# Kernel optimization log

Measured on AMD Instinct MI355X. Metric: run time of the kernel, lower is better.

Reference implementation:

```python
import jax, jax.numpy as jnp
import numpy as np

OVERLAP_THRESHOLD = 0.5
NEG_POS_RATIO = 3
ALPHA = 1.0


def cxcy_to_xy(cxcy):
    return jnp.concatenate([cxcy[..., :2] - cxcy[..., 2:] / 2,
                            cxcy[..., :2] + cxcy[..., 2:] / 2], axis=-1)


def xy_to_cxcy(xy):
    return jnp.concatenate([(xy[..., :2] + xy[..., 2:]) / 2,
                            xy[..., 2:] - xy[..., :2]], axis=-1)


def cxcy_to_gcxgcy(cxcy, priors_cxcy):
    return jnp.concatenate([
        (cxcy[..., :2] - priors_cxcy[..., :2]) / (priors_cxcy[..., 2:] / 10.0),
        jnp.log(cxcy[..., 2:] / priors_cxcy[..., 2:]) * 5.0], axis=-1)


def jaccard(a, b):
    # a: [N,4] xy, b: [P,4] xy -> [N,P]
    lo = jnp.maximum(a[:, None, :2], b[None, :, :2])
    hi = jnp.minimum(a[:, None, 2:], b[None, :, 2:])
    inter = jnp.prod(jnp.clip(hi - lo, 0.0), axis=-1)  # [N,P]
    area_a = jnp.prod(a[:, 2:] - a[:, :2], axis=-1)  # [N]
    area_b = jnp.prod(b[:, 2:] - b[:, :2], axis=-1)  # [P]
    return inter / (area_a[:, None] + area_b[None, :] - inter)


def _match_one(boxes_i, labels_i, priors_cxcy, priors_xy):
    n_objects = boxes_i.shape[0]
    overlap = jaccard(boxes_i, priors_xy)  # [N,P]
    overlap_for_each_prior = overlap.max(axis=0)  # [P]
    object_for_each_prior = overlap.argmax(axis=0)  # [P]
    prior_for_each_object = overlap.argmax(axis=1)  # [N]
    # force each object to own its best prior
    object_for_each_prior = object_for_each_prior.at[prior_for_each_object].set(
        jnp.arange(n_objects))
    overlap_for_each_prior = overlap_for_each_prior.at[prior_for_each_object].set(1.0)
    labels_for_each_prior = labels_i[object_for_each_prior]
    labels_for_each_prior = jnp.where(overlap_for_each_prior < OVERLAP_THRESHOLD,
                                      0, labels_for_each_prior)
    matched = boxes_i[object_for_each_prior]  # [P,4]
    true_locs = cxcy_to_gcxgcy(xy_to_cxcy(matched), priors_cxcy)  # [P,4]
    return true_locs, labels_for_each_prior


def reference(predicted_locs, predicted_scores, boxes, labels, priors_cxcy):
    B, P, C = predicted_scores.shape
    priors_xy = cxcy_to_xy(priors_cxcy)
    true_locs, true_classes = jax.vmap(
        _match_one, in_axes=(0, 0, None, None))(boxes, labels, priors_cxcy, priors_xy)
    # true_locs: [B,P,4], true_classes: [B,P]
    positive = true_classes != 0  # [B,P]
    n_pos = positive.sum(axis=1)  # [B]
    n_pos_total = n_pos.sum()

    # SmoothL1 (beta=1, mean over selected elements = n_pos_total*4)
    d = predicted_locs - true_locs
    ad = jnp.abs(d)
    sl1 = jnp.where(ad < 1.0, 0.5 * d * d, ad - 0.5)  # [B,P,4]
    loc_loss = (sl1 * positive[..., None]).sum() / (n_pos_total.astype(jnp.float32) * 4.0)

    # per-prior cross-entropy
    logp = jax.nn.log_softmax(predicted_scores, axis=-1)  # [B,P,C]
    conf_all = -jnp.take_along_axis(logp, true_classes[..., None], axis=-1)[..., 0]  # [B,P]

    conf_pos_sum = jnp.where(positive, conf_all, 0.0).sum()
    conf_neg = jnp.where(positive, 0.0, conf_all)
    conf_neg_sorted = jnp.sort(conf_neg, axis=1)[:, ::-1]  # descending
    n_hard_neg = NEG_POS_RATIO * n_pos  # [B]
    rank = jnp.arange(P)[None, :]
    hard_neg_mask = rank < n_hard_neg[:, None]
    conf_hard_neg_sum = jnp.where(hard_neg_mask, conf_neg_sorted, 0.0).sum()

    conf_loss = (conf_hard_neg_sum + conf_pos_sum) / n_pos_total.astype(jnp.float32)
    return conf_loss + ALPHA * loc_loss


def setup_inputs() -> dict:
    key = jax.random.key(0)
    ks = jax.random.split(key, 7)
    B, P, C, N = 128, 8732, 21, 16
    predicted_locs = jax.random.normal(ks[0], (B, P, 4), dtype=jnp.float32)
    predicted_scores = jax.random.normal(ks[1], (B, P, C), dtype=jnp.float32)
    # valid xy boxes in [0,1]
    p1 = jax.random.uniform(ks[2], (B, N, 2)) * 0.85
    wh = jax.random.uniform(ks[3], (B, N, 2), minval=0.02, maxval=0.15)
    boxes = jnp.concatenate([p1, jnp.minimum(p1 + wh, 1.0)], axis=-1)
    labels = jax.random.randint(ks[4], (B, N), 1, C)
    cxcy = jax.random.uniform(ks[5], (P, 2))
    pwh = jax.random.uniform(ks[6], (P, 2), minval=0.05, maxval=0.5)
    priors_cxcy = jnp.concatenate([cxcy, pwh], axis=-1)
    return {"predicted_locs": predicted_locs, "predicted_scores": predicted_scores,
            "boxes": boxes, "labels": labels, "priors_cxcy": priors_cxcy}
```

## Files before the change

### kernel.cpp

```cpp
#include <hip/hip_runtime.h>


#define MAXN 16
#define MAXE 16
#define SPLIT 8

__device__ __forceinline__ float sl1f(float d) {
    float ad = fabsf(d);
    return ad < 1.0f ? 0.5f * d * d : ad - 0.5f;
}

__global__ __launch_bounds__(256) void k_pre(
    const float* __restrict__ boxes,
    const float* __restrict__ priors,
    int P, int N,
    float* __restrict__ pf_in,
    float* __restrict__ pf_un,
    int*   __restrict__ pf_id,
    int* __restrict__ npos,
    float* __restrict__ acc)
{
    __shared__ float sbx1[MAXN], sby1[MAXN], sbx2[MAXN], sby2[MAXN], sba[MAXN];
    __shared__ float win[4][MAXN], wun[4][MAXN];
    __shared__ int   widd[4][MAXN];
    const int id = blockIdx.x;
    const int tid = threadIdx.x;
    const int lane = tid & 63, w = tid >> 6;
    const int b = id / SPLIT, s = id % SPLIT;

    if (s == 0 && tid == 0) npos[b] = 0;
    if (id == 0 && tid < 2) ((unsigned*)acc)[tid] = 0u;
    if (N > MAXN) N = MAXN;

    if (tid < N) {
        const float* bp = boxes + ((size_t)b * N + tid) * 4;
        float x1 = bp[0], y1 = bp[1], x2 = bp[2], y2 = bp[3];
        sbx1[tid] = x1; sby1[tid] = y1; sbx2[tid] = x2; sby2[tid] = y2;
        sba[tid] = (x2 - x1) * (y2 - y1);
    }
    __syncthreads();

    float rx1[MAXN], ry1[MAXN], rx2[MAXN], ry2[MAXN], rar[MAXN];
#pragma unroll
    for (int n = 0; n < MAXN; n++) {
        if (n < N) { rx1[n]=sbx1[n]; ry1[n]=sby1[n]; rx2[n]=sbx2[n]; ry2[n]=sby2[n]; rar[n]=sba[n]; }
        else       { rx1[n]=0.f; ry1[n]=0.f; rx2[n]=0.f; ry2[n]=0.f; rar[n]=0.f; }
    }

    const int Q = (P + SPLIT - 1) / SPLIT;
    const int pbeg = s * Q;
    const int pend = min(pbeg + Q, P);

    float bi[MAXN], bu[MAXN]; int bx[MAXN];
#pragma unroll
    for (int n = 0; n < MAXN; n++) { bi[n] = -1.0f; bu[n] = 1.0f; bx[n] = 0x7fffffff; }

    for (int p = pbeg + tid; p < pend; p += 256) {
        float4 pr = ((const float4*)priors)[p];
        float px1 = pr.x - pr.z * 0.5f, py1 = pr.y - pr.w * 0.5f;
        float px2 = pr.x + pr.z * 0.5f, py2 = pr.y + pr.w * 0.5f;
        float parea = (px2 - px1) * (py2 - py1);
#pragma unroll
        for (int n = 0; n < MAXN; n++) {
            if (n < N) {
                float iw = fmaxf(fminf(rx2[n], px2) - fmaxf(rx1[n], px1), 0.0f);
                float ih = fmaxf(fminf(ry2[n], py2) - fmaxf(ry1[n], py1), 0.0f);
                float in = iw * ih;
                float un = rar[n] + parea - in;
                if (in * bu[n] > bi[n] * un) { bi[n] = in; bu[n] = un; bx[n] = p; }
            }
        }
    }

#pragma unroll
    for (int n = 0; n < MAXN; n++) {
        if (n < N) {
#pragma unroll
            for (int off = 32; off > 0; off >>= 1) {
                float oin = __shfl_down(bi[n], off);
                float oun = __shfl_down(bu[n], off);
                int   oid = __shfl_down(bx[n], off);
                float a = oin * bu[n], c = bi[n] * oun;
                if (a > c || (a == c && oid < bx[n])) { bi[n] = oin; bu[n] = oun; bx[n] = oid; }
            }
            if (lane == 0) { win[w][n] = bi[n]; wun[w][n] = bu[n]; widd[w][n] = bx[n]; }
        }
    }
    __syncthreads();
    if (tid < N) {
        const int n = tid;
        float fi = win[0][n], fu = wun[0][n]; int fx = widd[0][n];
        for (int ww = 1; ww < 4; ww++) {
            float oin = win[ww][n], oun = wun[ww][n]; int oid = widd[ww][n];
            float a = oin * fu, c = fi * oun;
            if (a > c || (a == c && oid < fx)) { fi = oin; fu = oun; fx = oid; }
        }
        const size_t o = ((size_t)b * SPLIT + s) * MAXN + n;
        pf_in[o] = fi; pf_un[o] = fu; pf_id[o] = fx;
    }
}

template<int CT>
__global__ __launch_bounds__(256) void k_fused(
    const float* __restrict__ plocs,
    const float* __restrict__ scores,
    const float* __restrict__ boxes,
    const int*   __restrict__ labels,
    const float* __restrict__ priors,
    const float* __restrict__ pf_in,
    const float* __restrict__ pf_un,
    const int*   __restrict__ pf_id,
    int P, int Crt, int N, int nchunk,
    float* __restrict__ conf_out,
    int*   __restrict__ npos,
    float* __restrict__ locpart,
    float* __restrict__ pospart)
{
    const int C = CT > 0 ? CT : Crt;
    extern __shared__ float sh[];
    __shared__ float sx1[MAXN], sy1[MAXN], sx2[MAXN], sy2[MAXN], barea[MAXN];
    __shared__ int   blab[MAXN], spfo[MAXN];
    __shared__ float redf[4], redp[4];
    __shared__ int   redi[4];

    const int b = blockIdx.y;
    const int tid = threadIdx.x;
    const int lane = tid & 63, wid = tid >> 6;
    if (N > MAXN) N = MAXN;
    const int p0 = blockIdx.x * 256;
    const int rows = min(256, P - p0);

    if (tid < N) {
        const float* bp = boxes + ((size_t)b * N + tid) * 4;
        float x1 = bp[0], y1 = bp[1], x2 = bp[2], y2 = bp[3];
        sx1[tid] = x1; sy1[tid] = y1; sx2[tid] = x2; sy2[tid] = y2;
        barea[tid] = (x2 - x1) * (y2 - y1);
        blab[tid] = labels[(size_t)b * N + tid];
        const size_t base = (size_t)b * SPLIT * MAXN + tid;
        float fi = pf_in[base], fu = pf_un[base]; int fx = pf_id[base];
#pragma unroll
        for (int sp = 1; sp < SPLIT; sp++) {
            float oin = pf_in[base + (size_t)sp * MAXN];
            float oun = pf_un[base + (size_t)sp * MAXN];
            int   oid = pf_id[base + (size_t)sp * MAXN];
            if (oin * fu > fi * oun) { fi = oin; fu = oun; fx = oid; }
        }
        spfo[tid] = fx;
    }

    {
        const size_t f4base = ((size_t)b * P + p0) * C / 4;
        const int f4cnt = (rows * C + 3) / 4;
        const float4* __restrict__ s4 = (const float4*)scores + f4base;
        if ((P & 3) == 0) {
            for (int c = wid; c * 64 < f4cnt; c += 4) {
                int idx = c * 64 + lane;
                if (idx < f4cnt) {
                    __builtin_amdgcn_global_load_lds(
                        (const __attribute__((address_space(1))) void*)(s4 + idx),
                        (__attribute__((address_space(3))) void*)((char*)sh + (size_t)c * 1024),
                        16, 0, 0);
                }
            }
            asm volatile("s_waitcnt vmcnt(0)" ::: "memory");
        } else {
            for (int j = tid; j < f4cnt; j += 256)
                ((float4*)sh)[j] = s4[j];
        }
    }
    __syncthreads();

    const int p = p0 + tid;
    float locs = 0.0f, posc = 0.0f, conf = 0.0f;
    int np = 0;
    if (p < P) {
        float4 pr = ((const float4*)priors)[p];
        float px1 = pr.x - pr.z * 0.5f, py1 = pr.y - pr.w * 0.5f;
        float px2 = pr.x + pr.z * 0.5f, py2 = pr.y + pr.w * 0.5f;
        float parea = (px2 - px1) * (py2 - py1);
        float bi = -1.0f, bu = 1.0f; int bestn = 0;
#pragma unroll
        for (int n = 0; n < MAXN; n++) {
            if (n < N) {
                float iw = fmaxf(fminf(sx2[n], px2) - fmaxf(sx1[n], px1), 0.0f);
                float ih = fmaxf(fminf(sy2[n], py2) - fmaxf(sy1[n], py1), 0.0f);
                float in = iw * ih;
                float un = barea[n] + parea - in;
                if (in * bu > bi * un) { bi = in; bu = un; bestn = n; }
            }
        }
#pragma unroll
        for (int n = 0; n < MAXN; n++) {
            if (n < N && spfo[n] == p) { bestn = n; bi = 1.0f; bu = 1.0f; }
        }
        const int lab = (bi < 0.5f * bu) ? 0 : blab[bestn];

        const float* r = sh + tid * C;
        float m = -3.402823466e38f;
#pragma unroll
        for (int c = 0; c < C; c++) m = fmaxf(m, r[c]);
        float sum = 0.0f;
#pragma unroll
        for (int c = 0; c < C; c++) sum += __expf(r[c] - m);
        float ce = m + __logf(sum) - r[lab];

        if (lab != 0) {
            posc = ce; np = 1;
            int n = bestn;
            float cx = (sx1[n] + sx2[n]) * 0.5f, cy = (sy1[n] + sy2[n]) * 0.5f;
            float w = sx2[n] - sx1[n], h = sy2[n] - sy1[n];
            float g0 = (cx - pr.x) / (pr.z / 10.0f);
            float g1 = (cy - pr.y) / (pr.w / 10.0f);
            float g2 = logf(w / pr.z) * 5.0f;
            float g3 = logf(h / pr.w) * 5.0f;
            float4 pl = ((const float4*)plocs)[(size_t)b * P + p];
            locs = sl1f(pl.x - g0) + sl1f(pl.y - g1) + sl1f(pl.z - g2) + sl1f(pl.w - g3);
        } else {
            conf = ce;
        }
        conf_out[(size_t)b * P + p] = conf;
    }
#pragma unroll
    for (int off = 32; off > 0; off >>= 1) {
        locs += __shfl_down(locs, off);
        posc += __shfl_down(posc, off);
        np   += __shfl_down(np, off);
    }
    if (lane == 0) { redf[wid] = locs; redp[wid] = posc; redi[wid] = np; }
    __syncthreads();
    if (tid == 0) {
        float L = redf[0] + redf[1] + redf[2] + redf[3];
        float Pp = redp[0] + redp[1] + redp[2] + redp[3];
        int   c = redi[0] + redi[1] + redi[2] + redi[3];
        if (c) atomicAdd(&npos[b], c);
        locpart[b * nchunk + blockIdx.x] = L;
        pospart[b * nchunk + blockIdx.x] = Pp;
    }
}

__global__ __launch_bounds__(1024, 4) void k_hard(
    const float* __restrict__ conf,
    const int* __restrict__ npos,
    const float* __restrict__ locpart,
    const float* __restrict__ pospart,
    int P, int B, int nloc,
    float* __restrict__ acc,
    float* __restrict__ out)
{
    __shared__ int   redi[2][16 * 3];
    __shared__ float redf2[16];
    __shared__ int   redi2[16];
    __shared__ float rl[16], rp[16];
    __shared__ int   rn[16], is_last;
    const int b = blockIdx.x, tid = threadIdx.x;
    const int lane = tid & 63, wid = tid >> 6;
    const int nthr = blockDim.x, nw = nthr >> 6;
    const int ne = (P + nthr - 1) / nthr;
    long long kk = (long long)npos[b] * 3;
    int k = kk > P ? P : (int)kk;

    float S = 0.0f;
    if (k > 0) {
        unsigned e[MAXE];
#pragma unroll
        for (int j = 0; j < MAXE; j++) {
            int p = j * nthr + tid;
            e[j] = (j < ne && p < P) ? __float_as_uint(conf[(size_t)b * P + p]) : 0u;
        }

        unsigned lo = 0u, hi = 0x7F800000u;
        int itp = 0;
        while (lo < hi) {
            int* buf = redi[itp & 1]; itp++;
            unsigned span = hi - lo;
            if (span >= 8) {
                unsigned q = span >> 2;
                unsigned m1 = lo + q, m2 = lo + 2 * q, m3 = lo + 3 * q;
                int c1 = 0, c2 = 0, c3 = 0;
#pragma unroll
                for (int j = 0; j < MAXE; j++) {
                    if (j < ne) {
                        unsigned v = e[j];
                        c1 += (int)__popcll(__ballot(v >= m1));
                        c2 += (int)__popcll(__ballot(v >= m2));
                        c3 += (int)__popcll(__ballot(v >= m3));
                    }
                }
                if (lane == 0) {
                    buf[wid * 3 + 0] = c1; buf[wid * 3 + 1] = c2; buf[wid * 3 + 2] = c3;
                }
                __syncthreads();
                int C1 = 0, C2 = 0, C3 = 0;
                for (int w = 0; w < nw; w++) {
                    C1 += buf[w * 3 + 0]; C2 += buf[w * 3 + 1]; C3 += buf[w * 3 + 2];
                }
                if      (C3 >= k) lo = m3;
                else if (C2 >= k) { lo = m2; hi = m3 - 1; }
                else if (C1 >= k) { lo = m1; hi = m2 - 1; }
                else              hi = m1 - 1;
            } else {
                unsigned mid = lo + ((span + 1) >> 1);
                int c = 0;
#pragma unroll
                for (int j = 0; j < MAXE; j++)
                    if (j < ne) c += (int)__popcll(__ballot(e[j] >= mid));
                if (lane == 0) buf[wid * 3] = c;
                __syncthreads();
                int Cc = 0;
                for (int w = 0; w < nw; w++) Cc += buf[w * 3];
                if (Cc >= k) lo = mid; else hi = mid - 1;
            }
        }
        __syncthreads();

        float t = __uint_as_float(lo);
        float sgt = 0.0f; int cgt = 0;
#pragma unroll
        for (int j = 0; j < MAXE; j++) {
            if (j < ne) {
                float v = __uint_as_float(e[j]);
                if (v > t) { sgt += v; cgt++; }
            }
        }
#pragma unroll
        for (int off = 32; off > 0; off >>= 1) {
            sgt += __shfl_down(sgt, off);
            cgt += __shfl_down(cgt, off);
        }
        if (lane == 0) { redf2[wid] = sgt; redi2[wid] = cgt; }
        __syncthreads();
        if (tid == 0) {
            int Cg = 0;
            for (int w = 0; w < nw; w++) { S += redf2[w]; Cg += redi2[w]; }
            S += (float)(k - Cg) * t;
        }
        __syncthreads();
    }

    if (tid == 0) {
        atomicAdd(&acc[0], S);
        __threadfence();
        unsigned tk = atomicAdd((unsigned*)(acc + 1), 1u);
        is_last = (tk == (unsigned)gridDim.x - 1) ? 1 : 0;
    }
    __syncthreads();
    if (is_last) {
        float lp = 0.0f, pp = 0.0f; int np = 0;
        for (int i = tid; i < nloc; i += nthr) { lp += locpart[i]; pp += pospart[i]; }
        for (int i = tid; i < B; i += nthr) np += npos[i];
#pragma unroll
        for (int off = 32; off > 0; off >>= 1) {
            lp += __shfl_down(lp, off);
            pp += __shfl_down(pp, off);
            np += __shfl_down(np, off);
        }
        if (lane == 0) { rl[wid] = lp; rp[wid] = pp; rn[wid] = np; }
        __syncthreads();
        if (tid == 0) {
            float L = 0.0f, Pp = 0.0f; int Np = 0;
            for (int w = 0; w < nw; w++) { L += rl[w]; Pp += rp[w]; Np += rn[w]; }
            float hard = atomicAdd(&acc[0], 0.0f);
            float npf = (float)Np;
            out[0] = (hard + Pp) / npf + L / (npf * 4.0f);
        }
    }
}

extern "C" void kernel_launch(void* const* d_in, const int* in_sizes, int n_in,
                              void* d_out, int out_size, void* d_ws, size_t ws_size,
                              hipStream_t stream)
{
    const float* plocs  = (const float*)d_in[0];
    const float* scores = (const float*)d_in[1];
    const float* boxes  = (const float*)d_in[2];
    const int*   labels = (const int*)d_in[3];
    const float* priors = (const float*)d_in[4];

    int P = in_sizes[4] / 4;
    int B = in_sizes[0] / (P * 4);
    int C = in_sizes[1] / (in_sizes[0] / 4);
    int N = in_sizes[3] / B;
    int nchunk = (P + 255) / 256;
    int nloc = B * nchunk;

    char* w = (char*)d_ws;
    float* slot    = (float*)w;  w += (size_t)B * P * sizeof(float);
    int*   npos    = (int*)w;    w += (size_t)B * sizeof(int);
    float* pf_in   = (float*)w;  w += (size_t)B * SPLIT * MAXN * sizeof(float);
    float* pf_un   = (float*)w;  w += (size_t)B * SPLIT * MAXN * sizeof(float);
    int*   pf_id   = (int*)w;    w += (size_t)B * SPLIT * MAXN * sizeof(int);
    float* locpart = (float*)w;  w += (size_t)nloc * sizeof(float);
    float* pospart = (float*)w;  w += (size_t)nloc * sizeof(float);
    w = (char*)(((uintptr_t)w + 63) & ~(uintptr_t)63);
    float* acc     = (float*)w;

    k_pre<<<B * SPLIT, 256, 0, stream>>>(boxes, priors, P, N,
                                         pf_in, pf_un, pf_id, npos, acc);

    dim3 ga(nchunk, B);
    size_t smf = (size_t)256 * C * sizeof(float);
    if (C == 21) {
        k_fused<21><<<ga, 256, smf, stream>>>(plocs, scores, boxes, labels, priors,
                                              pf_in, pf_un, pf_id, P, C, N, nchunk,
                                              slot, npos, locpart, pospart);
    } else {
        k_fused<0><<<ga, 256, smf, stream>>>(plocs, scores, boxes, labels, priors,
                                             pf_in, pf_un, pf_id, P, C, N, nchunk,
                                             slot, npos, locpart, pospart);
    }

    k_hard<<<B, 1024, 0, stream>>>(slot, npos, locpart, pospart,
                                   P, B, nloc, acc, (float*)d_out);
}
```

Before: 231.3 us.

## Repartition prior-matching kernel across object pairs and prior halves

The prior-matching pre-kernel now parallelises over pairs of objects and two halves of the priors instead of all 16 objects across 8 prior splits. Each block keeps only 2 boxes in registers, which cuts register pressure and raises the block count from B*8 to B*16. The fused kernel now merges 2 partial results per object instead of 8. Separately, the hard-negative threshold search drops its double-buffered reduction scratch in favour of one buffer with an extra barrier per iteration, which adds synchronisation cost.

```diff
diff --git a/kernel.cpp b/kernel.cpp
--- a/kernel.cpp
+++ b/kernel.cpp
@@ -3,7 +3,8 @@
 
 #define MAXN 16
 #define MAXE 16
-#define SPLIT 8
+#define KP_NB 2
+#define KP_SP 2
 
 __device__ __forceinline__ float sl1f(float d) {
     float ad = fabsf(d);
@@ -13,90 +14,87 @@
 __global__ __launch_bounds__(256) void k_pre(
     const float* __restrict__ boxes,
     const float* __restrict__ priors,
-    int P, int N,
+    int P, int N, int npair,
     float* __restrict__ pf_in,
     float* __restrict__ pf_un,
     int*   __restrict__ pf_id,
     int* __restrict__ npos,
     float* __restrict__ acc)
 {
-    __shared__ float sbx1[MAXN], sby1[MAXN], sbx2[MAXN], sby2[MAXN], sba[MAXN];
-    __shared__ float win[4][MAXN], wun[4][MAXN];
-    __shared__ int   widd[4][MAXN];
+    __shared__ float win[4][KP_NB], wun[4][KP_NB];
+    __shared__ int   widd[4][KP_NB];
     const int id = blockIdx.x;
     const int tid = threadIdx.x;
     const int lane = tid & 63, w = tid >> 6;
-    const int b = id / SPLIT, s = id % SPLIT;
-
-    if (s == 0 && tid == 0) npos[b] = 0;
+    const int per_b = npair * KP_SP;
+    const int b = id / per_b, rem = id % per_b;
+    const int pr = rem / KP_SP, h = rem % KP_SP;
+    const int n0 = pr * KP_NB;
+    const int nb = min(KP_NB, N - n0);
+
+    if (tid == 0 && rem == 0) npos[b] = 0;
     if (id == 0 && tid < 2) ((unsigned*)acc)[tid] = 0u;
-    if (N > MAXN) N = MAXN;
-
-    if (tid < N) {
-        const float* bp = boxes + ((size_t)b * N + tid) * 4;
-        float x1 = bp[0], y1 = bp[1], x2 = bp[2], y2 = bp[3];
-        sbx1[tid] = x1; sby1[tid] = y1; sbx2[tid] = x2; sby2[tid] = y2;
-        sba[tid] = (x2 - x1) * (y2 - y1);
+
+    float rx1[KP_NB], ry1[KP_NB], rx2[KP_NB], ry2[KP_NB], rar[KP_NB];
+#pragma unroll
+    for (int j = 0; j < KP_NB; j++) {
+        const int n = n0 + (j < nb ? j : 0);
+        const float* bp = boxes + ((size_t)b * N + n) * 4;
+        rx1[j] = bp[0]; ry1[j] = bp[1]; rx2[j] = bp[2]; ry2[j] = bp[3];
+        rar[j] = (rx2[j] - rx1[j]) * (ry2[j] - ry1[j]);
+    }
+
+    const int Q = (P + KP_SP - 1) / KP_SP;
+    const int pbeg = h * Q;
+    const int pend = min(pbeg + Q, P);
+
+    float bi[KP_NB], bu[KP_NB]; int bx[KP_NB];
+#pragma unroll
+    for (int j = 0; j < KP_NB; j++) { bi[j] = -1.0f; bu[j] = 1.0f; bx[j] = 0x7fffffff; }
+
+#pragma unroll 2
+    for (int p = pbeg + tid; p < pend; p += 256) {
+        float4 prr = ((const float4*)priors)[p];
+        float px1 = prr.x - prr.z * 0.5f, py1 = prr.y - prr.w * 0.5f;
+        float px2 = prr.x + prr.z * 0.5f, py2 = prr.y + prr.w * 0.5f;
+        float parea = (px2 - px1) * (py2 - py1);
+#pragma unroll
+        for (int j = 0; j < KP_NB; j++) {
+            float iw = fmaxf(fminf(rx2[j], px2) - fmaxf(rx1[j], px1), 0.0f);
+            float ih = fmaxf(fminf(ry2[j], py2) - fmaxf(ry1[j], py1), 0.0f);
+            float in = iw * ih;
+            float un = rar[j] + parea - in;
+            if (in * bu[j] > bi[j] * un) { bi[j] = in; bu[j] = un; bx[j] = p; }
+        }
+    }
+
+#pragma unroll
+    for (int j = 0; j < KP_NB; j++) {
+#pragma unroll
+        for (int off = 32; off > 0; off >>= 1) {
+            float oin = __shfl_down(bi[j], off);
+            float oun = __shfl_down(bu[j], off);
+            int   oid = __shfl_down(bx[j], off);
+            float a = oin * bu[j], c = bi[j] * oun;
+            if (a > c || (a == c && oid < bx[j])) { bi[j] = oin; bu[j] = oun; bx[j] = oid; }
+        }
+        if (lane == 0) { win[w][j] = bi[j]; wun[w][j] = bu[j]; widd[w][j] = bx[j]; }
     }
     __syncthreads();
-
-    float rx1[MAXN], ry1[MAXN], rx2[MAXN], ry2[MAXN], rar[MAXN];
-#pragma unroll
-    for (int n = 0; n < MAXN; n++) {
-        if (n < N) { rx1[n]=sbx1[n]; ry1[n]=sby1[n]; rx2[n]=sbx2[n]; ry2[n]=sby2[n]; rar[n]=sba[n]; }
-        else       { rx1[n]=0.f; ry1[n]=0.f; rx2[n]=0.f; ry2[n]=0.f; rar[n]=0.f; }
-    }
-
-    const int Q = (P + SPLIT - 1) / SPLIT;
-    const int pbeg = s * Q;
-    const int pend = min(pbeg + Q, P);
-
-    float bi[MAXN], bu[MAXN]; int bx[MAXN];
-#pragma unroll
-    for (int n = 0; n < MAXN; n++) { bi[n] = -1.0f; bu[n] = 1.0f; bx[n] = 0x7fffffff; }
-
-    for (int p = pbeg + tid; p < pend; p += 256) {
-        float4 pr = ((const float4*)priors)[p];
-        float px1 = pr.x - pr.z * 0.5f, py1 = pr.y - pr.w * 0.5f;
-        float px2 = pr.x + pr.z * 0.5f, py2 = pr.y + pr.w * 0.5f;
-        float parea = (px2 - px1) * (py2 - py1);
-#pragma unroll
-        for (int n = 0; n < MAXN; n++) {
-            if (n < N) {
-                float iw = fmaxf(fminf(rx2[n], px2) - fmaxf(rx1[n], px1), 0.0f);
-                float ih = fmaxf(fminf(ry2[n], py2) - fmaxf(ry1[n], py1), 0.0f);
-                float in = iw * ih;
-                float un = rar[n] + parea - in;
-                if (in * bu[n] > bi[n] * un) { bi[n] = in; bu[n] = un; bx[n] = p; }
-            }
-        }
-    }
-
-#pragma unroll
-    for (int n = 0; n < MAXN; n++) {
-        if (n < N) {
-#pragma unroll
-            for (int off = 32; off > 0; off >>= 1) {
-                float oin = __shfl_down(bi[n], off);
-                float oun = __shfl_down(bu[n], off);
-                int   oid = __shfl_down(bx[n], off);
-                float a = oin * bu[n], c = bi[n] * oun;
-                if (a > c || (a == c && oid < bx[n])) { bi[n] = oin; bu[n] = oun; bx[n] = oid; }
-            }
-            if (lane == 0) { win[w][n] = bi[n]; wun[w][n] = bu[n]; widd[w][n] = bx[n]; }
-        }
-    }
-    __syncthreads();
-    if (tid < N) {
-        const int n = tid;
-        float fi = win[0][n], fu = wun[0][n]; int fx = widd[0][n];
-        for (int ww = 1; ww < 4; ww++) {
-            float oin = win[ww][n], oun = wun[ww][n]; int oid = widd[ww][n];
-            float a = oin * fu, c = fi * oun;
-            if (a > c || (a == c && oid < fx)) { fi = oin; fu = oun; fx = oid; }
-        }
-        const size_t o = ((size_t)b * SPLIT + s) * MAXN + n;
-        pf_in[o] = fi; pf_un[o] = fu; pf_id[o] = fx;
+    if (tid == 0) {
+#pragma unroll
+        for (int j = 0; j < KP_NB; j++) {
+            float fi = win[0][j], fu = wun[0][j]; int fx = widd[0][j];
+            for (int ww = 1; ww < 4; ww++) {
+                float oin = win[ww][j], oun = wun[ww][j]; int oid = widd[ww][j];
+                float a = oin * fu, c = fi * oun;
+                if (a > c || (a == c && oid < fx)) { fi = oin; fu = oun; fx = oid; }
+            }
+            if (j < nb) {
+                const size_t o = ((size_t)b * KP_SP + h) * MAXN + n0 + j;
+                pf_in[o] = fi; pf_un[o] = fu; pf_id[o] = fx;
+            }
+        }
     }
 }
 
@@ -136,10 +134,10 @@
         sx1[tid] = x1; sy1[tid] = y1; sx2[tid] = x2; sy2[tid] = y2;
         barea[tid] = (x2 - x1) * (y2 - y1);
         blab[tid] = labels[(size_t)b * N + tid];
-        const size_t base = (size_t)b * SPLIT * MAXN + tid;
+        const size_t base = (size_t)b * KP_SP * MAXN + tid;
         float fi = pf_in[base], fu = pf_un[base]; int fx = pf_id[base];
 #pragma unroll
-        for (int sp = 1; sp < SPLIT; sp++) {
+        for (int sp = 1; sp < KP_SP; sp++) {
             float oin = pf_in[base + (size_t)sp * MAXN];
             float oun = pf_un[base + (size_t)sp * MAXN];
             int   oid = pf_id[base + (size_t)sp * MAXN];
@@ -247,7 +245,7 @@
     float* __restrict__ acc,
     float* __restrict__ out)
 {
-    __shared__ int   redi[2][16 * 3];
+    __shared__ int   redi[16 * 3];
     __shared__ float redf2[16];
     __shared__ int   redi2[16];
     __shared__ float rl[16], rp[16];
@@ -269,9 +267,7 @@
         }
 
         unsigned lo = 0u, hi = 0x7F800000u;
-        int itp = 0;
         while (lo < hi) {
-            int* buf = redi[itp & 1]; itp++;
             unsigned span = hi - lo;
             if (span >= 8) {
                 unsigned q = span >> 2;
@@ -287,13 +283,14 @@
                     }
                 }
                 if (lane == 0) {
-                    buf[wid * 3 + 0] = c1; buf[wid * 3 + 1] = c2; buf[wid * 3 + 2] = c3;
+                    redi[wid * 3 + 0] = c1; redi[wid * 3 + 1] = c2; redi[wid * 3 + 2] = c3;
                 }
                 __syncthreads();
                 int C1 = 0, C2 = 0, C3 = 0;
                 for (int w = 0; w < nw; w++) {
-                    C1 += buf[w * 3 + 0]; C2 += buf[w * 3 + 1]; C3 += buf[w * 3 + 2];
+                    C1 += redi[w * 3 + 0]; C2 += redi[w * 3 + 1]; C3 += redi[w * 3 + 2];
                 }
+                __syncthreads();
                 if      (C3 >= k) lo = m3;
                 else if (C2 >= k) { lo = m2; hi = m3 - 1; }
                 else if (C1 >= k) { lo = m1; hi = m2 - 1; }
@@ -304,14 +301,14 @@
 #pragma unroll
                 for (int j = 0; j < MAXE; j++)
                     if (j < ne) c += (int)__popcll(__ballot(e[j] >= mid));
-                if (lane == 0) buf[wid * 3] = c;
+                if (lane == 0) redi[wid * 3] = c;
                 __syncthreads();
                 int Cc = 0;
-                for (int w = 0; w < nw; w++) Cc += buf[w * 3];
+                for (int w = 0; w < nw; w++) Cc += redi[w * 3];
+                __syncthreads();
                 if (Cc >= k) lo = mid; else hi = mid - 1;
             }
         }
-        __syncthreads();
 
         float t = __uint_as_float(lo);
         float sgt = 0.0f; int cgt = 0;
@@ -382,20 +379,21 @@
     int N = in_sizes[3] / B;
     int nchunk = (P + 255) / 256;
     int nloc = B * nchunk;
+    int npair = (N + KP_NB - 1) / KP_NB;
 
     char* w = (char*)d_ws;
     float* slot    = (float*)w;  w += (size_t)B * P * sizeof(float);
     int*   npos    = (int*)w;    w += (size_t)B * sizeof(int);
-    float* pf_in   = (float*)w;  w += (size_t)B * SPLIT * MAXN * sizeof(float);
-    float* pf_un   = (float*)w;  w += (size_t)B * SPLIT * MAXN * sizeof(float);
-    int*   pf_id   = (int*)w;    w += (size_t)B * SPLIT * MAXN * sizeof(int);
+    float* pf_in   = (float*)w;  w += (size_t)B * KP_SP * MAXN * sizeof(float);
+    float* pf_un   = (float*)w;  w += (size_t)B * KP_SP * MAXN * sizeof(float);
+    int*   pf_id   = (int*)w;    w += (size_t)B * KP_SP * MAXN * sizeof(int);
     float* locpart = (float*)w;  w += (size_t)nloc * sizeof(float);
     float* pospart = (float*)w;  w += (size_t)nloc * sizeof(float);
     w = (char*)(((uintptr_t)w + 63) & ~(uintptr_t)63);
     float* acc     = (float*)w;
 
-    k_pre<<<B * SPLIT, 256, 0, stream>>>(boxes, priors, P, N,
-                                         pf_in, pf_un, pf_id, npos, acc);
+    k_pre<<<B * npair * KP_SP, 256, 0, stream>>>(boxes, priors, P, N, npair,
+                                                 pf_in, pf_un, pf_id, npos, acc);
 
     dim3 ga(nchunk, B);
     size_t smf = (size_t)256 * C * sizeof(float);
```

Result: faster. 207.4 us (-10.3%).
